# Kernel tuning notes

Measured on AMD Instinct MI355X. Metric: run time of the kernel, lower is better.

## Reference

```python
import jax, jax.numpy as jnp
import numpy as np

N_NODES = 50000
N_EDGES = 800000
HIDDEN = 256
LAYERS = 10


def setup_inputs() -> dict:
    key = jax.random.key(0)
    ks = jax.random.split(key, 8)
    x = jax.random.normal(ks[0], (N_NODES, 1), dtype=jnp.float32)
    edge_index = jax.random.randint(ks[1], (2, N_EDGES), 0, N_NODES, dtype=jnp.int64)
    # GCNConv weights (Glorot-ish scale)
    W1 = jax.random.normal(ks[2], (1, HIDDEN), dtype=jnp.float32) * (1.0 / np.sqrt(1))
    b1 = jnp.zeros((HIDDEN,), dtype=jnp.float32)
    W = jax.random.normal(ks[3], (HIDDEN, HIDDEN), dtype=jnp.float32) * (1.0 / np.sqrt(HIDDEN))
    b = jnp.zeros((HIDDEN,), dtype=jnp.float32)
    Wc = jax.random.normal(ks[4], (HIDDEN, 1), dtype=jnp.float32) * (1.0 / np.sqrt(HIDDEN))
    bc = jnp.zeros((1,), dtype=jnp.float32)
    return {"x": x, "edge_index": edge_index, "W1": W1, "b1": b1,
            "W": W, "b": b, "Wc": Wc, "bc": bc}


def _gcn_norm(edge_index, n_nodes):
    # PyG GCNConv default: add self-loops, symmetric normalization
    loop = jnp.arange(n_nodes, dtype=edge_index.dtype)
    src = jnp.concatenate([edge_index[0], loop])
    dst = jnp.concatenate([edge_index[1], loop])
    ones = jnp.ones(src.shape[0], dtype=jnp.float32)
    deg = jax.ops.segment_sum(ones, dst, num_segments=n_nodes)
    dinv = jnp.where(deg > 0, jax.lax.rsqrt(deg), 0.0)
    norm = dinv[src] * dinv[dst]  # [E+N]
    return src, dst, norm


def _gcn_conv(h, W, b, src, dst, norm, n_nodes):
    h = h @ W                                   # [N, H] dense transform first (small GEMM)
    msg = h[src] * norm[:, None]                # gather + scale  [E+N, H]
    out = jax.ops.segment_sum(msg, dst, num_segments=n_nodes)  # scatter-add
    return out + b


def reference(x, edge_index, W1, b1, W, b, Wc, bc):
    n = x.shape[0]
    src, dst, norm = _gcn_norm(edge_index, n)  # graph is static across layers
    h = jax.nn.relu(_gcn_conv(x, W1, b1, src, dst, norm, n))
    for _ in range(1, LAYERS):  # layers 1..9 share the same weights (self.conv reused)
        h = jax.nn.relu(_gcn_conv(h, W, b, src, dst, norm, n))
    return h @ Wc + bc  # [N, 1]
```

## Files before the change

### kernel.cpp

```cpp
#include <hip/hip_runtime.h>

typedef long long ll;
typedef __attribute__((ext_vector_type(8))) short short8;
typedef __attribute__((ext_vector_type(4))) float f32x4;
constexpr int HID = 256;
constexpr int LDSS = 264;

__device__ inline ushort f2bf(float f){
  uint u = __float_as_uint(f);
  u += 0x7FFFu + ((u >> 16) & 1u);
  return (ushort)(u >> 16);
}

__global__ void k_diag(float* out, int n, float val){
  int i = blockIdx.x*256 + threadIdx.x;
  if (i < n) out[i] = val;
}

__global__ void k_detect(const int* ei, int* flag){
  __shared__ int bad;
  if (threadIdx.x == 0) bad = 0;
  __syncthreads();
  for (int i = threadIdx.x; i < 2048; i += 256)
    if (ei[2*i+1] != 0) bad = 1;
  __syncthreads();
  if (threadIdx.x == 0) *flag = bad ? 0 : 1;
}

__global__ void k_count(const int* ei, ll E, const int* flag, int* cnt){
  ll i = (ll)blockIdx.x*256 + threadIdx.x;
  if (i >= E) return;
  int f = *flag;
  int d = f ? (int)((const ll*)ei)[E + i] : ei[E + i];
  atomicAdd(&cnt[d], 1);
}

__global__ void k_scan_a(const int* __restrict__ cnt, int* __restrict__ bsum, int n){
  __shared__ int s[256];
  int t = threadIdx.x, i = blockIdx.x*256 + t;
  s[t] = (i < n) ? cnt[i] : 0;
  __syncthreads();
  for (int off = 128; off; off >>= 1){
    if (t < off) s[t] += s[t + off];
    __syncthreads();
  }
  if (t == 0) bsum[blockIdx.x] = s[0];
}

__global__ void k_scan_b(const int* __restrict__ bsum, int* __restrict__ boff,
                         int nb, int* __restrict__ row_ptr, int n){
  __shared__ int s[256];
  int t = threadIdx.x;
  int v = (t < nb) ? bsum[t] : 0;
  s[t] = v; __syncthreads();
  for (int off = 1; off < 256; off <<= 1){
    int add = (t >= off) ? s[t - off] : 0;
    __syncthreads();
    s[t] += add;
    __syncthreads();
  }
  if (t < nb) boff[t] = s[t] - v;
  if (t == nb - 1) row_ptr[n] = s[t];
}

__global__ void k_scan_c(const int* __restrict__ cnt, const int* __restrict__ boff,
                         int* __restrict__ row_ptr, int n){
  __shared__ int s[256];
  int t = threadIdx.x, i = blockIdx.x*256 + t;
  int v = (i < n) ? cnt[i] : 0;
  s[t] = v; __syncthreads();
  for (int off = 1; off < 256; off <<= 1){
    int add = (t >= off) ? s[t - off] : 0;
    __syncthreads();
    s[t] += add;
    __syncthreads();
  }
  if (i < n) row_ptr[i] = boff[blockIdx.x] + s[t] - v;
}

__global__ void k_dinv(const int* cnt, const float* x, float* dinv, float* xd, int n){
  int i = blockIdx.x*256 + threadIdx.x;
  if (i >= n) return;
  float dv = 1.0f / sqrtf((float)(cnt[i] + 1));
  dinv[i] = dv;
  xd[i] = x[i] * dv;
}

__global__ void k_place(const int* ei, ll E, const int* flag, int* fill, int* col){
  ll i = (ll)blockIdx.x*256 + threadIdx.x;
  if (i >= E) return;
  int f = *flag;
  int s, d;
  if (f){ const ll* e64 = (const ll*)ei; s = (int)e64[i]; d = (int)e64[E + i]; }
  else  { s = ei[i]; d = ei[E + i]; }
  int p = atomicAdd(&fill[d], 1);
  col[p] = s;
}

__global__ void k_layer1(const float* __restrict__ xd, const int* __restrict__ row_ptr,
                         const int* __restrict__ col, float* __restrict__ g, int n){
  int i = blockIdx.x*256 + threadIdx.x;
  if (i >= n) return;
  float s = xd[i];
  int e0 = row_ptr[i], e1 = row_ptr[i+1];
  for (int e = e0; e < e1; ++e) s += xd[col[e]];
  g[i] = s;
}

__global__ void k_splitW(const float* __restrict__ W, short* __restrict__ Bt){
  int idx = blockIdx.x*256 + threadIdx.x;
  if (idx >= 16*8*64) return;
  int nb = idx >> 9, kc = (idx >> 6) & 7, l = idx & 63;
  short8 hi, lo;
  #pragma unroll
  for (int j = 0; j < 8; ++j){
    int k = kc*32 + ((l >> 4) * 8) + j;
    int c = nb*16 + (l & 15);
    float wv = W[k*HID + c];
    ushort h = f2bf(wv);
    float hf = __uint_as_float((uint)h << 16);
    hi[j] = (short)h;
    lo[j] = (short)f2bf(wv - hf);
  }
  ((short8*)Bt)[idx] = hi;
  ((short8*)Bt)[8192 + idx] = lo;
}

template<int MODE>
__global__ __launch_bounds__(256, 4) void k_gemm_mfma(
  const void* __restrict__ Ain, const short* __restrict__ Bt,
  const float* __restrict__ bias, const float* __restrict__ W1,
  const float* __restrict__ dinv, ushort* __restrict__ ts_bf, int n)
{
  __shared__ short Ah[64*LDSS];
  int t = threadIdx.x;
  int r0 = blockIdx.x * 64;

  #pragma unroll
  for (int i = 0; i < 8; ++i){
    int id  = i*256 + t;
    int row = id >> 5;
    int c16 = id & 31;
    int v   = r0 + row;
    short8 hi8 = {0,0,0,0,0,0,0,0};
    if (v < n){
      if (MODE == 0){
        float gv = dinv[v] * ((const float*)Ain)[v];
        const float4* wp = (const float4*)(W1 + c16*8);
        const float4* bp = (const float4*)(bias + c16*8);
        float4 w0 = wp[0], w1 = wp[1], b0 = bp[0], b1 = bp[1];
        hi8[0] = (short)f2bf(fmaxf(fmaf(gv,w0.x,b0.x), 0.f));
        hi8[1] = (short)f2bf(fmaxf(fmaf(gv,w0.y,b0.y), 0.f));
        hi8[2] = (short)f2bf(fmaxf(fmaf(gv,w0.z,b0.z), 0.f));
        hi8[3] = (short)f2bf(fmaxf(fmaf(gv,w0.w,b0.w), 0.f));
        hi8[4] = (short)f2bf(fmaxf(fmaf(gv,w1.x,b1.x), 0.f));
        hi8[5] = (short)f2bf(fmaxf(fmaf(gv,w1.y,b1.y), 0.f));
        hi8[6] = (short)f2bf(fmaxf(fmaf(gv,w1.z,b1.z), 0.f));
        hi8[7] = (short)f2bf(fmaxf(fmaf(gv,w1.w,b1.w), 0.f));
      } else {
        hi8 = ((const short8*)Ain)[(size_t)v*32 + c16];
      }
    }
    *(short8*)&Ah[row*LDSS + c16*8] = hi8;
  }
  __syncthreads();

  int l = t & 63, w = t >> 6;
  const short8* Btv = (const short8*)Bt;
  f32x4 acc[4][4];
  #pragma unroll
  for (int m = 0; m < 4; ++m)
    #pragma unroll
    for (int nf = 0; nf < 4; ++nf)
      acc[m][nf] = (f32x4){0.f,0.f,0.f,0.f};

  for (int kc = 0; kc < 8; ++kc){
    short8 ah[4];
    #pragma unroll
    for (int m = 0; m < 4; ++m){
      int row = m*16 + (l & 15);
      ah[m] = *(const short8*)&Ah[row*LDSS + (kc*4 + (l >> 4))*8];
    }
    #pragma unroll
    for (int nf = 0; nf < 4; ++nf){
      int nb = w*4 + nf;
      short8 bh = Btv[(size_t)(nb*8 + kc)*64 + l];
      short8 bl = Btv[(size_t)8192 + (nb*8 + kc)*64 + l];
      #pragma unroll
      for (int m = 0; m < 4; ++m){
        acc[m][nf] = __builtin_amdgcn_mfma_f32_16x16x32_bf16(ah[m], bh, acc[m][nf], 0,0,0);
        acc[m][nf] = __builtin_amdgcn_mfma_f32_16x16x32_bf16(ah[m], bl, acc[m][nf], 0,0,0);
      }
    }
  }

  #pragma unroll
  for (int m = 0; m < 4; ++m){
    int rowb = r0 + m*16 + ((l >> 4)*4);
    #pragma unroll
    for (int r = 0; r < 4; ++r){
      int v = rowb + r;
      if (v < n){
        float dv = dinv[v];
        #pragma unroll
        for (int nf = 0; nf < 4; ++nf){
          int colb = w*64 + nf*16 + (l & 15);
          ts_bf[(size_t)v*HID + colb] = f2bf(dv * acc[m][nf][r]);
        }
      }
    }
  }
}

__device__ inline void bfacc(uint2 u, float4& a){
  a.x += __uint_as_float(u.x << 16);
  a.y += __uint_as_float(u.x & 0xFFFF0000u);
  a.z += __uint_as_float(u.y << 16);
  a.w += __uint_as_float(u.y & 0xFFFF0000u);
}

__global__ __launch_bounds__(256, 4) void k_scatter_bf(
  const ushort* __restrict__ ts_bf, const int* __restrict__ row_ptr,
  const int* __restrict__ col, const float* __restrict__ bias,
  const float* __restrict__ dinv, ushort* __restrict__ Abf, int n)
{
  int w = (int)((blockIdx.x*256 + threadIdx.x) >> 6);
  int lane = threadIdx.x & 63;
  if (w >= n) return;
  const uint2* tsp = ((const uint2*)ts_bf) + lane;
  int e0 = row_ptr[w], e1 = row_ptr[w+1];

  float4 a0 = make_float4(0.f,0.f,0.f,0.f);
  float4 a1 = make_float4(0.f,0.f,0.f,0.f);
  float4 a2 = make_float4(0.f,0.f,0.f,0.f);
  float4 a3 = make_float4(0.f,0.f,0.f,0.f);
  bfacc(tsp[(size_t)w*64], a0);

  int e = e0;
  for (; e + 4 <= e1; e += 4){
    int c0 = col[e+0], c1 = col[e+1], c2 = col[e+2], c3 = col[e+3];
    uint2 v0 = tsp[(size_t)c0*64];
    uint2 v1 = tsp[(size_t)c1*64];
    uint2 v2 = tsp[(size_t)c2*64];
    uint2 v3 = tsp[(size_t)c3*64];
    bfacc(v0, a0); bfacc(v1, a1); bfacc(v2, a2); bfacc(v3, a3);
  }
  for (; e < e1; ++e){
    uint2 v = tsp[(size_t)col[e]*64];
    bfacc(v, a0);
  }

  a0.x += a1.x + a2.x + a3.x;
  a0.y += a1.y + a2.y + a3.y;
  a0.z += a1.z + a2.z + a3.z;
  a0.w += a1.w + a2.w + a3.w;

  float dv = dinv[w];
  float4 bb = ((const float4*)bias)[lane];
  uint2 o;
  o.x = (uint)f2bf(fmaxf(fmaf(dv, a0.x, bb.x), 0.f))
      | ((uint)f2bf(fmaxf(fmaf(dv, a0.y, bb.y), 0.f)) << 16);
  o.y = (uint)f2bf(fmaxf(fmaf(dv, a0.z, bb.z), 0.f))
      | ((uint)f2bf(fmaxf(fmaf(dv, a0.w, bb.w), 0.f)) << 16);
  ((uint2*)Abf)[(size_t)w*64 + lane] = o;
}

__global__ __launch_bounds__(256) void k_out(
  const ushort* __restrict__ Abf, const float* __restrict__ Wc,
  const float* __restrict__ bc, float* __restrict__ out, int n)
{
  int w = (int)((blockIdx.x*256 + threadIdx.x) >> 6);
  int lane = threadIdx.x & 63;
  if (w >= n) return;
  uint2 u = ((const uint2*)Abf)[(size_t)w*64 + lane];
  float4 wc = ((const float4*)Wc)[lane];
  float s = __uint_as_float(u.x << 16)          * wc.x
          + __uint_as_float(u.x & 0xFFFF0000u)  * wc.y
          + __uint_as_float(u.y << 16)          * wc.z
          + __uint_as_float(u.y & 0xFFFF0000u)  * wc.w;
  #pragma unroll
  for (int off = 32; off; off >>= 1) s += __shfl_down(s, off, 64);
  if (lane == 0) out[w] = s + bc[0];
}

extern "C" void kernel_launch(void* const* d_in, const int* in_sizes, int n_in,
                              void* d_out, int out_size, void* d_ws, size_t ws_size,
                              hipStream_t stream)
{
  const float* x  = (const float*)d_in[0];
  const int*   ei = (const int*)d_in[1];
  const float* W1 = (const float*)d_in[2];
  const float* b1 = (const float*)d_in[3];
  const float* Wm = (const float*)d_in[4];
  const float* bm = (const float*)d_in[5];
  const float* Wc = (const float*)d_in[6];
  const float* bc = (const float*)d_in[7];
  float* out = (float*)d_out;
  const int N = in_sizes[0];
  const ll  E = in_sizes[1] / 2;

  char* ws = (char*)d_ws;
  size_t off = 0;
  auto carve = [&](size_t bytes)->char*{
    char* p = ws + off; off += (bytes + 255) & ~(size_t)255; return p;
  };
  int*   cnt     = (int*)  carve((size_t)N*4);
  int*   row_ptr = (int*)  carve((size_t)(N+1)*4);
  int*   fill    = (int*)  carve((size_t)N*4);
  float* dinv    = (float*)carve((size_t)N*4);
  float* xd      = (float*)carve((size_t)N*4);
  float* g       = (float*)carve((size_t)N*4);
  int*   flag    = (int*)  carve(256);
  int*   bsum    = (int*)  carve(1024);
  int*   boff    = (int*)  carve(1024);
  short* Bt      = (short*)carve((size_t)2*8192*8*2);
  int*   col     = (int*)  carve((size_t)E*4);
  ushort* ts_bf  = (ushort*)carve((size_t)N*HID*2);
  ushort* Abf    = (ushort*)carve((size_t)N*HID*2);
  if (off > ws_size){
    k_diag<<<(out_size+255)/256, 256, 0, stream>>>(out, out_size, (float)(ws_size >> 20));
    return;
  }

  hipMemsetAsync(cnt, 0, (size_t)N*4, stream);
  k_detect<<<1, 256, 0, stream>>>(ei, flag);
  int eblocks = (int)((E + 255) / 256);
  k_count<<<eblocks, 256, 0, stream>>>(ei, E, flag, cnt);
  int nb = (N + 255) / 256;
  k_scan_a<<<nb, 256, 0, stream>>>(cnt, bsum, N);
  k_scan_b<<<1, 256, 0, stream>>>(bsum, boff, nb, row_ptr, N);
  k_scan_c<<<nb, 256, 0, stream>>>(cnt, boff, row_ptr, N);
  k_dinv<<<(N+255)/256, 256, 0, stream>>>(cnt, x, dinv, xd, N);
  hipMemcpyAsync(fill, row_ptr, (size_t)N*4, hipMemcpyDeviceToDevice, stream);
  k_place<<<eblocks, 256, 0, stream>>>(ei, E, flag, fill, col);
  k_splitW<<<32, 256, 0, stream>>>(Wm, Bt);
  k_layer1<<<(N+255)/256, 256, 0, stream>>>(xd, row_ptr, col, g, N);

  int gblocks = (N + 63) / 64;
  int sblocks = (N + 3) / 4;
  k_gemm_mfma<0><<<gblocks, 256, 0, stream>>>(g, Bt, b1, W1, dinv, ts_bf, N);
  k_scatter_bf<<<sblocks, 256, 0, stream>>>(ts_bf, row_ptr, col, bm, dinv, Abf, N);
  for (int l = 0; l < 8; ++l){
    k_gemm_mfma<1><<<gblocks, 256, 0, stream>>>(Abf, Bt, bm, nullptr, dinv, ts_bf, N);
    k_scatter_bf<<<sblocks, 256, 0, stream>>>(ts_bf, row_ptr, col, bm, dinv, Abf, N);
  }
  k_out<<<sblocks, 256, 0, stream>>>(Abf, Wc, bc, out, N);
}
```

Before: 868.1 us.

## Store node features in column-sliced layout so scatter gathers stay cache-resident

Feature tensors between the GEMM and the scatter are now stored as 8 column slices of 32 bf16 each, [slice][node][32], instead of row-major [node][256]. The scatter kernel gives each block one slice, with 8 lanes per node and 32 nodes per block, so each slice (about 3.2 MB) can stay in cache while the random neighbour gathers run. The GEMM load and store and the output kernel are changed to match the new layout, and the column-index loads are marked nontemporal. The cost is that col and row_ptr are now read eight times per layer, and each gather is a narrower 64-byte segment per node.

```diff
diff --git a/kernel.cpp b/kernel.cpp
--- a/kernel.cpp
+++ b/kernel.cpp
@@ -138,13 +138,13 @@
 
   #pragma unroll
   for (int i = 0; i < 8; ++i){
-    int id  = i*256 + t;
-    int row = id >> 5;
-    int c16 = id & 31;
-    int v   = r0 + row;
-    short8 hi8 = {0,0,0,0,0,0,0,0};
-    if (v < n){
-      if (MODE == 0){
+    if (MODE == 0){
+      int id  = i*256 + t;
+      int row = id >> 5;
+      int c16 = id & 31;
+      int v   = r0 + row;
+      short8 hi8 = {0,0,0,0,0,0,0,0};
+      if (v < n){
         float gv = dinv[v] * ((const float*)Ain)[v];
         const float4* wp = (const float4*)(W1 + c16*8);
         const float4* bp = (const float4*)(bias + c16*8);
@@ -157,11 +157,16 @@
         hi8[5] = (short)f2bf(fmaxf(fmaf(gv,w1.y,b1.y), 0.f));
         hi8[6] = (short)f2bf(fmaxf(fmaf(gv,w1.z,b1.z), 0.f));
         hi8[7] = (short)f2bf(fmaxf(fmaf(gv,w1.w,b1.w), 0.f));
-      } else {
-        hi8 = ((const short8*)Ain)[(size_t)v*32 + c16];
       }
+      *(short8*)&Ah[row*LDSS + c16*8] = hi8;
+    } else {
+      int row = t >> 2, off = t & 3;
+      int v = r0 + row;
+      short8 hi8 = {0,0,0,0,0,0,0,0};
+      if (v < n)
+        hi8 = ((const short8*)Ain)[(size_t)i*n*4 + (size_t)v*4 + off];
+      *(short8*)&Ah[row*LDSS + (i*4 + off)*8] = hi8;
     }
-    *(short8*)&Ah[row*LDSS + c16*8] = hi8;
   }
   __syncthreads();
 
@@ -205,7 +210,8 @@
         #pragma unroll
         for (int nf = 0; nf < 4; ++nf){
           int colb = w*64 + nf*16 + (l & 15);
-          ts_bf[(size_t)v*HID + colb] = f2bf(dv * acc[m][nf][r]);
+          int slice = colb >> 5, within = colb & 31;
+          ts_bf[(size_t)slice*n*32 + (size_t)v*32 + within] = f2bf(dv * acc[m][nf][r]);
         }
       }
     }
@@ -219,34 +225,40 @@
   a.w += __uint_as_float(u.y & 0xFFFF0000u);
 }
 
-__global__ __launch_bounds__(256, 4) void k_scatter_bf(
+__global__ __launch_bounds__(256, 4) void k_scatter_sl(
   const ushort* __restrict__ ts_bf, const int* __restrict__ row_ptr,
   const int* __restrict__ col, const float* __restrict__ bias,
   const float* __restrict__ dinv, ushort* __restrict__ Abf, int n)
 {
-  int w = (int)((blockIdx.x*256 + threadIdx.x) >> 6);
-  int lane = threadIdx.x & 63;
-  if (w >= n) return;
-  const uint2* tsp = ((const uint2*)ts_bf) + lane;
-  int e0 = row_ptr[w], e1 = row_ptr[w+1];
+  int b = blockIdx.x;
+  int s = b & 7;
+  int t = threadIdx.x;
+  int node = (b >> 3)*32 + (t >> 3);
+  int lin = t & 7;
+  if (node >= n) return;
+  const uint2* tsp = (const uint2*)ts_bf + (size_t)s*n*8 + lin;
+  int e0 = row_ptr[node], e1 = row_ptr[node+1];
 
   float4 a0 = make_float4(0.f,0.f,0.f,0.f);
   float4 a1 = make_float4(0.f,0.f,0.f,0.f);
   float4 a2 = make_float4(0.f,0.f,0.f,0.f);
   float4 a3 = make_float4(0.f,0.f,0.f,0.f);
-  bfacc(tsp[(size_t)w*64], a0);
+  bfacc(tsp[(size_t)node*8], a0);
 
   int e = e0;
   for (; e + 4 <= e1; e += 4){
-    int c0 = col[e+0], c1 = col[e+1], c2 = col[e+2], c3 = col[e+3];
-    uint2 v0 = tsp[(size_t)c0*64];
-    uint2 v1 = tsp[(size_t)c1*64];
-    uint2 v2 = tsp[(size_t)c2*64];
-    uint2 v3 = tsp[(size_t)c3*64];
+    int c0 = __builtin_nontemporal_load(col + e + 0);
+    int c1 = __builtin_nontemporal_load(col + e + 1);
+    int c2 = __builtin_nontemporal_load(col + e + 2);
+    int c3 = __builtin_nontemporal_load(col + e + 3);
+    uint2 v0 = tsp[(size_t)c0*8];
+    uint2 v1 = tsp[(size_t)c1*8];
+    uint2 v2 = tsp[(size_t)c2*8];
+    uint2 v3 = tsp[(size_t)c3*8];
     bfacc(v0, a0); bfacc(v1, a1); bfacc(v2, a2); bfacc(v3, a3);
   }
   for (; e < e1; ++e){
-    uint2 v = tsp[(size_t)col[e]*64];
+    uint2 v = tsp[(size_t)__builtin_nontemporal_load(col + e)*8];
     bfacc(v, a0);
   }
 
@@ -255,14 +267,14 @@
   a0.z += a1.z + a2.z + a3.z;
   a0.w += a1.w + a2.w + a3.w;
 
-  float dv = dinv[w];
-  float4 bb = ((const float4*)bias)[lane];
+  float dv = dinv[node];
+  float4 bb = *(const float4*)(bias + s*32 + lin*4);
   uint2 o;
   o.x = (uint)f2bf(fmaxf(fmaf(dv, a0.x, bb.x), 0.f))
       | ((uint)f2bf(fmaxf(fmaf(dv, a0.y, bb.y), 0.f)) << 16);
   o.y = (uint)f2bf(fmaxf(fmaf(dv, a0.z, bb.z), 0.f))
       | ((uint)f2bf(fmaxf(fmaf(dv, a0.w, bb.w), 0.f)) << 16);
-  ((uint2*)Abf)[(size_t)w*64 + lane] = o;
+  ((uint2*)Abf)[(size_t)s*n*8 + (size_t)node*8 + lin] = o;
 }
 
 __global__ __launch_bounds__(256) void k_out(
@@ -272,7 +284,7 @@
   int w = (int)((blockIdx.x*256 + threadIdx.x) >> 6);
   int lane = threadIdx.x & 63;
   if (w >= n) return;
-  uint2 u = ((const uint2*)Abf)[(size_t)w*64 + lane];
+  uint2 u = ((const uint2*)Abf)[(size_t)(lane >> 3)*n*8 + (size_t)w*8 + (lane & 7)];
   float4 wc = ((const float4*)Wc)[lane];
   float s = __uint_as_float(u.x << 16)          * wc.x
           + __uint_as_float(u.x & 0xFFFF0000u)  * wc.y
@@ -337,12 +349,13 @@
   k_layer1<<<(N+255)/256, 256, 0, stream>>>(xd, row_ptr, col, g, N);
 
   int gblocks = (N + 63) / 64;
-  int sblocks = (N + 3) / 4;
+  int sblocks = 8 * ((N + 31) / 32);
+  int oblocks = (N + 3) / 4;
   k_gemm_mfma<0><<<gblocks, 256, 0, stream>>>(g, Bt, b1, W1, dinv, ts_bf, N);
-  k_scatter_bf<<<sblocks, 256, 0, stream>>>(ts_bf, row_ptr, col, bm, dinv, Abf, N);
+  k_scatter_sl<<<sblocks, 256, 0, stream>>>(ts_bf, row_ptr, col, bm, dinv, Abf, N);
   for (int l = 0; l < 8; ++l){
     k_gemm_mfma<1><<<gblocks, 256, 0, stream>>>(Abf, Bt, bm, nullptr, dinv, ts_bf, N);
-    k_scatter_bf<<<sblocks, 256, 0, stream>>>(ts_bf, row_ptr, col, bm, dinv, Abf, N);
-  }
-  k_out<<<sblocks, 256, 0, stream>>>(Abf, Wc, bc, out, N);
-}
+    k_scatter_sl<<<sblocks, 256, 0, stream>>>(ts_bf, row_ptr, col, bm, dinv, Abf, N);
+  }
+  k_out<<<oblocks, 256, 0, stream>>>(Abf, Wc, bc, out, N);
+}
```

Result: slower. 1.132 ms (+30.5%).
